# Kernel tuning notes

Measured on AMD Instinct MI355X. Metric: run time of the kernel, lower is better.

The kernel has to match this reference:

```python
import jax, jax.numpy as jnp
import numpy as np

B, C, L = 8, 64, 16384
IN, H = 64, 32


def _lstm_dir(x, wih, whh, bih, bhh):
    """Single-direction LSTM, PyTorch gate order (i, f, g, o).
    x: [B, L, H] -> hidden outputs [B, L, H]."""
    xt = jnp.transpose(x, (1, 0, 2))  # [L, B, H]
    # Precompute input contributions for all timesteps (one big GEMM).
    xg = jnp.einsum('lbh,gh->lbg', xt, wih) + bih + bhh  # [L, B, 4H]
    h0 = jnp.zeros((x.shape[0], H), x.dtype)
    c0 = jnp.zeros((x.shape[0], H), x.dtype)

    def step(carry, xg_t):
        h, c = carry
        gates = xg_t + h @ whh.T  # [B, 4H]
        i, f, g, o = jnp.split(gates, 4, axis=-1)
        i = jax.nn.sigmoid(i)
        f = jax.nn.sigmoid(f)
        g = jnp.tanh(g)
        o = jax.nn.sigmoid(o)
        c = f * c + i * g
        h = o * jnp.tanh(c)
        return (h, c), h

    _, hs = jax.lax.scan(step, (h0, c0), xg)  # hs: [L, B, H]
    return jnp.transpose(hs, (1, 0, 2))


def setup_inputs() -> dict:
    key = jax.random.key(0)
    ks = jax.random.split(key, 24)
    u = lambda k, shape, bound: jax.random.uniform(k, shape, jnp.float32, -bound, bound)
    kp = 1.0 / np.sqrt(IN)
    kh = 1.0 / np.sqrt(H)
    k2 = 1.0 / np.sqrt(2 * H)
    return {
        'x': jax.random.normal(ks[0], (B, C, L), jnp.float32),
        'proj_w': u(ks[1], (H, IN), kp), 'proj_b': u(ks[2], (H,), kp),
        'wih_f': u(ks[3], (4 * H, H), kh), 'whh_f': u(ks[4], (4 * H, H), kh),
        'bih_f': u(ks[5], (4 * H,), kh), 'bhh_f': u(ks[6], (4 * H,), kh),
        'wih_b': u(ks[7], (4 * H, H), kh), 'whh_b': u(ks[8], (4 * H, H), kh),
        'bih_b': u(ks[9], (4 * H,), kh), 'bhh_b': u(ks[10], (4 * H,), kh),
        'bc_w1': u(ks[11], (H, 2 * H), k2), 'bc_b1': u(ks[12], (H,), k2),
        'bc_w2': u(ks[13], (1, H), kh), 'bc_b2': u(ks[14], (1,), kh),
        'rc_w1': u(ks[15], (H, 2 * H), k2), 'rc_b1': u(ks[16], (H,), k2),
        'rc_w2': u(ks[17], (1, H), kh), 'rc_b2': u(ks[18], (1,), kh),
        'is_sequence': 1,
    }


def _forward(x, proj_w, proj_b, wih_f, whh_f, bih_f, bhh_f, wih_b, whh_b, bih_b, bhh_b, bc_w1, bc_b1, bc_w2, bc_b2, rc_w1, rc_b1, rc_w2, rc_b2):
    x_seq = jnp.transpose(x, (0, 2, 1))  # [B, L, C]
    projected = x_seq @ proj_w.T + proj_b  # [B, L, H]
    h_fwd = _lstm_dir(projected, wih_f, whh_f, bih_f, bhh_f)
    h_bwd = _lstm_dir(projected[:, ::-1, :], wih_b, whh_b, bih_b, bhh_b)[:, ::-1, :]
    lstm_out = jnp.concatenate([h_fwd, h_bwd], axis=-1)  # [B, L, 2H]
    # boundary classifier (Linear-ReLU-Linear-Sigmoid)
    hid = jax.nn.relu(lstm_out @ bc_w1.T + bc_b1)
    probs = jax.nn.sigmoid(hid @ bc_w2.T + bc_b2)[..., 0]  # [B, L]
    # vectorized boundary-adjust stencil (replaces the O(B*L) python loop)
    lg = probs[:, 1:-1] - probs[:, :-2]
    rg = probs[:, 1:-1] - probs[:, 2:]
    inner = jnp.where((lg < 0) & (jnp.abs(lg) > jnp.abs(rg)), -1.0,
                      jnp.where((rg < 0) & (jnp.abs(rg) > jnp.abs(lg)), 1.0, 0.0))
    adj = jnp.pad(inner.astype(probs.dtype), ((0, 0), (1, 1)))  # [B, L]
    # real classifier on mean-pooled lstm output
    pooled = lstm_out.mean(axis=1)  # [B, 2H]
    rhid = jax.nn.relu(pooled @ rc_w1.T + rc_b1)
    real = jax.nn.sigmoid(rhid @ rc_w2.T + rc_b2)  # [B, 1]
    return probs, adj, real


def reference(x, proj_w, proj_b, wih_f, whh_f, bih_f, bhh_f, wih_b, whh_b, bih_b, bhh_b, bc_w1, bc_b1, bc_w2, bc_b2, rc_w1, rc_b1, rc_w2, rc_b2, is_sequence):
    assert is_sequence  # this reference implements the is_sequence=True path
    return _forward(x, proj_w, proj_b, wih_f, whh_f, bih_f, bhh_f, wih_b, whh_b, bih_b, bhh_b, bc_w1, bc_b1, bc_w2, bc_b2, rc_w1, rc_b1, rc_w2, rc_b2)
```

## Files before the change

### kernel.cpp

```cpp
#include <hip/hip_runtime.h>

#define LSEQ 16384
#define BB 8

__device__ __forceinline__ float rcp_f(float x) { return __builtin_amdgcn_rcpf(x); }
__device__ __forceinline__ float sig_f(float x) { return rcp_f(1.f + __expf(-x)); }
__device__ __forceinline__ float rdlane(float v, int k) {
  return __int_as_float(__builtin_amdgcn_readlane(__float_as_int(v), k));
}

__device__ __forceinline__ float swap_hi(float a, float b) {
  auto r = __builtin_amdgcn_permlane32_swap(__float_as_uint(a), __float_as_uint(b), false, false);
  unsigned out[2];
  __builtin_memcpy(out, &r, 8);
  return __uint_as_float(out[1]);
}

#define PIN16(w) asm volatile("" \
  : "+v"((w)[0]), "+v"((w)[1]), "+v"((w)[2]),  "+v"((w)[3]),  \
    "+v"((w)[4]), "+v"((w)[5]), "+v"((w)[6]),  "+v"((w)[7]),  \
    "+v"((w)[8]), "+v"((w)[9]), "+v"((w)[10]), "+v"((w)[11]), \
    "+v"((w)[12]),"+v"((w)[13]),"+v"((w)[14]), "+v"((w)[15]))

__global__ __launch_bounds__(256) void k0_weights(
    const float* __restrict__ proj_w, const float* __restrict__ proj_b,
    const float* __restrict__ wih_f, const float* __restrict__ bih_f, const float* __restrict__ bhh_f,
    const float* __restrict__ wih_b, const float* __restrict__ bih_b, const float* __restrict__ bhh_b,
    float* __restrict__ Wc, float* __restrict__ Wbias) {
  int G = threadIdx.x;
  int d = G >> 7, g = G & 127;
  const float* wih = d ? wih_b : wih_f;
  const float* bih = d ? bih_b : bih_f;
  const float* bhh = d ? bhh_b : bhh_f;
  float wr[32];
  #pragma unroll
  for (int k = 0; k < 32; k += 4) {
    float4 a = *(const float4*)(wih + g * 32 + k);
    wr[k] = a.x; wr[k + 1] = a.y; wr[k + 2] = a.z; wr[k + 3] = a.w;
  }
  for (int c = 0; c < 64; ++c) {
    float s = 0.f;
    #pragma unroll
    for (int k = 0; k < 32; ++k) s = fmaf(wr[k], proj_w[k * 64 + c], s);
    Wc[c * 256 + G] = s;
  }
  float s = bih[g] + bhh[g];
  #pragma unroll
  for (int k = 0; k < 32; ++k) s = fmaf(wr[k], proj_b[k], s);
  Wbias[G] = s;
}

__global__ __launch_bounds__(256) void k1_xg(
    const float* __restrict__ x, const float* __restrict__ Wc, const float* __restrict__ Wbias,
    float* __restrict__ xg, int dsel) {
  __shared__ float lds[64 * 132];
  int tid = threadIdx.x;
  int b = blockIdx.x >> 7;
  int t0 = (blockIdx.x & 127) << 7;
  #pragma unroll
  for (int i = 0; i < 8; ++i) {
    int slot = tid + (i << 8);
    int c = slot >> 5, u4 = slot & 31;
    float4 v = *(const float4*)(x + (size_t)(b * 64 + c) * LSEQ + t0 + u4 * 4);
    *(float4*)&lds[c * 128 + u4 * 4] = v;
  }
  __syncthreads();
  int lane = tid & 63;
  int w = tid >> 6;
  int th = w >> 1;
  int tl = (th << 6) + lane;
  int gb = (w & 1) << 6;
  int gcol = __builtin_amdgcn_readfirstlane(dsel * 128 + gb);
  float acc[64];
  #pragma unroll
  for (int gg = 0; gg < 64; ++gg) acc[gg] = 0.f;
  for (int c = 0; c < 64; ++c) {
    float xv = lds[c * 128 + tl];
    #pragma unroll
    for (int gg = 0; gg < 64; ++gg)
      acc[gg] = fmaf(Wc[c * 256 + gcol + gg], xv, acc[gg]);
  }
  #pragma unroll
  for (int p = 0; p < 2; ++p) {
    __syncthreads();
    if (th == p) {
      #pragma unroll
      for (int gg = 0; gg < 64; ++gg)
        lds[(tl & 63) * 132 + gb + gg] = acc[gg] + Wbias[gcol + gg];
    }
    __syncthreads();
    float* dst = xg + (size_t)(b * LSEQ + t0 + (p << 6)) * 128;
    #pragma unroll
    for (int k = 0; k < 8; ++k) {
      int f = (tid << 2) + (k << 10);
      int trow = f >> 7, g = f & 127;
      *(float4*)(dst + f) = *(const float4*)&lds[trow * 132 + g];
    }
  }
}

template<int DIR>
__device__ __forceinline__ void scan_chunk(const float* __restrict__ whh,
                                           const float* __restrict__ xg,
                                           float* __restrict__ hbuf,
                                           int lane, int ci) {
  const int g0 = (lane < 32) ? lane : lane + 32;
  const int g1 = g0 + 32;
  float w0[32], w1[32];
  #pragma unroll
  for (int k = 0; k < 32; ++k) {
    w0[k] = whh[g0 * 32 + k];
    w1[k] = whh[g1 * 32 + k];
  }
  const float M0 = (lane < 32) ? -1.f : -2.f;
  const float S0 = (lane < 32) ? 1.f : 2.f;
  const float D0 = (lane < 32) ? 0.f : -1.f;

  const int sOwn = ci << 6;
  const int s0 = (ci == 0) ? 0 : (sOwn - 64);
  const int ow = sOwn - s0;
  const int nblk = ((sOwn + 64) - s0) >> 3;

  constexpr int ST = DIR ? -128 : 128;
  constexpr int SH = DIR ? -32 : 32;
  const float* pld = xg + (size_t)(DIR ? (LSEQ - 1 - s0) : s0) * 128;
  float* ph = hbuf + (size_t)(DIR ? (LSEQ - 1 - s0) : s0) * 32;

  float nx0[8], nx1[8];
  #pragma unroll
  for (int j = 0; j < 8; ++j) {
    nx0[j] = pld[j * ST + g0];
    nx1[j] = pld[j * ST + g1];
  }
  pld += 8 * ST;

  float h = 0.f, c = 0.f;

#define STEP(j, PREFETCH, GUARD)                                           \
  {                                                                        \
    PIN16(w0); PIN16(w0 + 16); PIN16(w1); PIN16(w1 + 16);                  \
    float c0a = nx0[j], c1a = nx1[j];                                      \
    if (PREFETCH) {                                                        \
      nx0[j] = pld[(j) * ST + g0];                                         \
      nx1[j] = pld[(j) * ST + g1];                                         \
    }                                                                      \
    float c0b = 0.f, c1b = 0.f;                                            \
    _Pragma("unroll")                                                      \
    for (int k = 0; k < 16; ++k) {                                         \
      float hA = rdlane(h, k);                                             \
      float hB = rdlane(h, k + 16);                                        \
      c0a = fmaf(hA, w0[k], c0a);                                          \
      c1a = fmaf(hA, w1[k], c1a);                                          \
      c0b = fmaf(hB, w0[k + 16], c0b);                                     \
      c1b = fmaf(hB, w1[k + 16], c1b);                                     \
    }                                                                      \
    float gx = c0a + c0b;                                                  \
    float gy = c1a + c1b;                                                  \
    float y0 = fmaf(S0, rcp_f(1.f + __expf(gx * M0)), D0);                 \
    float y1 = rcp_f(1.f + __expf(-gy));                                   \
    float b0 = swap_hi(y0, y1);                                            \
    float b1 = swap_hi(y1, y1);                                            \
    c = fmaf(y1, c, y0 * b0);                                              \
    float tc = fmaf(2.f, rcp_f(1.f + __expf(-2.f * c)), -1.f);             \
    h = b1 * tc;                                                           \
    if (GUARD) { if (lane < 32) ph[(j) * SH + lane] = h; }                 \
  }

  for (int blk = 0; blk < nblk - 1; ++blk) {
    const int sb = blk << 3;
    #pragma unroll
    for (int j = 0; j < 8; ++j) {
      STEP(j, true, sb + j >= ow);
    }
    pld += 8 * ST;
    ph += 8 * SH;
  }
  #pragma unroll
  for (int j = 0; j < 8; ++j) {
    STEP(j, false, true);
  }
#undef STEP
}

template<int DIR>
__global__ __launch_bounds__(64, 1) void k2_scan(
    const float* __restrict__ whh, const float* __restrict__ xg,
    float* __restrict__ hbuf) {
  const int lane = threadIdx.x;
  const int b = blockIdx.x >> 8;
  const int ci = blockIdx.x & 255;
  scan_chunk<DIR>(whh, xg + (size_t)b * LSEQ * 128, hbuf + (size_t)b * LSEQ * 32, lane, ci);
}

__global__ __launch_bounds__(256) void k3_probs(
    const float* __restrict__ hF, const float* __restrict__ hB,
    const float* __restrict__ w1, const float* __restrict__ b1,
    const float* __restrict__ w2, const float* __restrict__ b2,
    float* __restrict__ out, float* __restrict__ pooledP) {
  __shared__ float red[256 * 65];
  int b = blockIdx.x >> 6;
  int tile = blockIdx.x & 63;
  int t = (tile << 8) + threadIdx.x;
  const float* hf = hF + (size_t)(b * LSEQ + t) * 32;
  const float* hb = hB + (size_t)(b * LSEQ + t) * 32;
  float v[64];
  #pragma unroll
  for (int i = 0; i < 8; ++i) {
    float4 a = *(const float4*)(hf + i * 4);
    v[i * 4] = a.x; v[i * 4 + 1] = a.y; v[i * 4 + 2] = a.z; v[i * 4 + 3] = a.w;
    float4 bb = *(const float4*)(hb + i * 4);
    v[32 + i * 4] = bb.x; v[32 + i * 4 + 1] = bb.y; v[32 + i * 4 + 2] = bb.z; v[32 + i * 4 + 3] = bb.w;
  }
  float tot = b2[0];
  for (int j = 0; j < 32; ++j) {
    float s = b1[j];
    #pragma unroll
    for (int g = 0; g < 64; ++g) s = fmaf(w1[j * 64 + g], v[g], s);
    tot = fmaf(w2[j], fmaxf(s, 0.f), tot);
  }
  out[(size_t)b * LSEQ + t] = sig_f(tot);
  #pragma unroll
  for (int g = 0; g < 64; ++g) red[threadIdx.x * 65 + g] = v[g];
  __syncthreads();
  if (threadIdx.x < 64) {
    int g = threadIdx.x;
    float s = 0.f;
    for (int tt = 0; tt < 256; ++tt) s += red[tt * 65 + g];
    pooledP[(b * 64 + tile) * 64 + g] = s;
  }
}

__global__ __launch_bounds__(512) void k45_tail(
    const float* __restrict__ probs, const float* __restrict__ pooledP,
    const float* __restrict__ rw1, const float* __restrict__ rb1,
    const float* __restrict__ rw2, const float* __restrict__ rb2,
    float* __restrict__ adj, float* __restrict__ out_real) {
  __shared__ float pm[512];
  __shared__ float rh[256];
  int tid = threadIdx.x;
  if (blockIdx.x < 256) {
    int i = blockIdx.x * 512 + tid;
    int t = i & (LSEQ - 1);
    float v = 0.f;
    if (t > 0 && t < LSEQ - 1) {
      float pmv = probs[i - 1], p = probs[i], pp = probs[i + 1];
      float lg = p - pmv, rg = p - pp;
      float al = fabsf(lg), ar = fabsf(rg);
      if (lg < 0.f && al > ar) v = -1.f;
      else if (rg < 0.f && ar > al) v = 1.f;
    }
    adj[i] = v;
  } else {
    {
      int b = tid >> 6, g = tid & 63;
      float s = 0.f;
      for (int ch = 0; ch < 64; ++ch) s += pooledP[(b * 64 + ch) * 64 + g];
      pm[b * 64 + g] = s * (1.f / LSEQ);
    }
    __syncthreads();
    if (tid < 256) {
      int b = tid >> 5, j = tid & 31;
      float s = rb1[j];
      #pragma unroll
      for (int g = 0; g < 64; ++g) s = fmaf(rw1[j * 64 + g], pm[b * 64 + g], s);
      rh[b * 32 + j] = fmaxf(s, 0.f);
    }
    __syncthreads();
    if (tid < 8) {
      float s = rb2[0];
      #pragma unroll
      for (int j = 0; j < 32; ++j) s = fmaf(rw2[j], rh[tid * 32 + j], s);
      out_real[tid] = sig_f(s);
    }
  }
}

extern "C" void kernel_launch(void* const* d_in, const int* in_sizes, int n_in,
                              void* d_out, int out_size, void* d_ws, size_t ws_size,
                              hipStream_t stream) {
  const float* x      = (const float*)d_in[0];
  const float* proj_w = (const float*)d_in[1];
  const float* proj_b = (const float*)d_in[2];
  const float* wih_f  = (const float*)d_in[3];
  const float* whh_f  = (const float*)d_in[4];
  const float* bih_f  = (const float*)d_in[5];
  const float* bhh_f  = (const float*)d_in[6];
  const float* wih_b  = (const float*)d_in[7];
  const float* whh_b  = (const float*)d_in[8];
  const float* bih_b  = (const float*)d_in[9];
  const float* bhh_b  = (const float*)d_in[10];
  const float* bc_w1  = (const float*)d_in[11];
  const float* bc_b1  = (const float*)d_in[12];
  const float* bc_w2  = (const float*)d_in[13];
  const float* bc_b2  = (const float*)d_in[14];
  const float* rc_w1  = (const float*)d_in[15];
  const float* rc_b1  = (const float*)d_in[16];
  const float* rc_w2  = (const float*)d_in[17];
  const float* rc_b2  = (const float*)d_in[18];

  float* ws = (float*)d_ws;
  float* xg = ws;
  float* hF = xg + (size_t)BB * LSEQ * 128;
  float* hB = hF + (size_t)BB * LSEQ * 32;
  float* Wc = hB + (size_t)BB * LSEQ * 32;
  float* Wbias = Wc + 64 * 256;
  float* pooledP = Wbias + 256;

  float* out = (float*)d_out;
  float* probs = out;
  float* adj = out + BB * LSEQ;
  float* real = out + 2 * BB * LSEQ;

  hipLaunchKernelGGL(k0_weights, dim3(1), dim3(256), 0, stream,
                     proj_w, proj_b, wih_f, bih_f, bhh_f, wih_b, bih_b, bhh_b, Wc, Wbias);
  hipLaunchKernelGGL(k1_xg, dim3(BB * 128), dim3(256), 0, stream, x, Wc, Wbias, xg, 0);
  hipLaunchKernelGGL((k2_scan<0>), dim3(BB * 256), dim3(64), 0, stream, whh_f, xg, hF);
  hipLaunchKernelGGL(k1_xg, dim3(BB * 128), dim3(256), 0, stream, x, Wc, Wbias, xg, 1);
  hipLaunchKernelGGL((k2_scan<1>), dim3(BB * 256), dim3(64), 0, stream, whh_b, xg, hB);

  hipLaunchKernelGGL(k3_probs, dim3(BB * 64), dim3(256), 0, stream,
                     hF, hB, bc_w1, bc_b1, bc_w2, bc_b2, probs, pooledP);
  hipLaunchKernelGGL(k45_tail, dim3(257), dim3(512), 0, stream,
                     probs, pooledP, rc_w1, rc_b1, rc_w2, rc_b2, adj, real);
}
```

Measured before the change: 243.7 us.

## Run both LSTM directions concurrently and use 128-step scan chunks

Gives each direction its own input-gate buffer when the workspace is large enough. The forward and backward projection GEMMs then run as one 2048-block launch, and both direction scans run as one 2048-block launch, replacing four serialized launches. Each scan block now owns 128 timesteps instead of 64, still with a 64-step warmup, so the total redundant warmup work drops by half. The cost is lower per-direction block counts, longer sequential chains per block, and double the xg workspace; a fallback path keeps the old serialized schedule when the workspace is small.

New measurement: 246.4 us. No clear change (+1.1%).

```diff
diff --git a/kernel.cpp b/kernel.cpp
--- a/kernel.cpp
+++ b/kernel.cpp
@@ -52,11 +52,13 @@
 
 __global__ __launch_bounds__(256) void k1_xg(
     const float* __restrict__ x, const float* __restrict__ Wc, const float* __restrict__ Wbias,
-    float* __restrict__ xg, int dsel) {
+    float* __restrict__ xgF, float* __restrict__ xgB, int dselBase) {
   __shared__ float lds[64 * 132];
   int tid = threadIdx.x;
-  int b = blockIdx.x >> 7;
-  int t0 = (blockIdx.x & 127) << 7;
+  int dsel = (int)(blockIdx.x >> 10) | dselBase;
+  int bi = blockIdx.x & 1023;
+  int b = bi >> 7;
+  int t0 = (bi & 127) << 7;
   #pragma unroll
   for (int i = 0; i < 8; ++i) {
     int slot = tid + (i << 8);
@@ -80,6 +82,7 @@
     for (int gg = 0; gg < 64; ++gg)
       acc[gg] = fmaf(Wc[c * 256 + gcol + gg], xv, acc[gg]);
   }
+  float* xg = dsel ? xgB : xgF;
   #pragma unroll
   for (int p = 0; p < 2; ++p) {
     __syncthreads();
@@ -116,10 +119,10 @@
   const float S0 = (lane < 32) ? 1.f : 2.f;
   const float D0 = (lane < 32) ? 0.f : -1.f;
 
-  const int sOwn = ci << 6;
+  const int sOwn = ci << 7;
   const int s0 = (ci == 0) ? 0 : (sOwn - 64);
   const int ow = sOwn - s0;
-  const int nblk = ((sOwn + 64) - s0) >> 3;
+  const int nblk = ((sOwn + 128) - s0) >> 3;
 
   constexpr int ST = DIR ? -128 : 128;
   constexpr int SH = DIR ? -32 : 32;
@@ -182,14 +185,19 @@
 #undef STEP
 }
 
-template<int DIR>
-__global__ __launch_bounds__(64, 1) void k2_scan(
-    const float* __restrict__ whh, const float* __restrict__ xg,
-    float* __restrict__ hbuf) {
+__global__ __launch_bounds__(64, 1) void k2_dual(
+    const float* __restrict__ whh_f, const float* __restrict__ whh_b,
+    const float* __restrict__ xgF, const float* __restrict__ xgB,
+    float* __restrict__ hF, float* __restrict__ hB, int dirBase) {
   const int lane = threadIdx.x;
-  const int b = blockIdx.x >> 8;
-  const int ci = blockIdx.x & 255;
-  scan_chunk<DIR>(whh, xg + (size_t)b * LSEQ * 128, hbuf + (size_t)b * LSEQ * 32, lane, ci);
+  const int dir = (int)(blockIdx.x >> 10) + dirBase;
+  const int inner = blockIdx.x & 1023;
+  const int b = inner >> 7;
+  const int ci = inner & 127;
+  if (dir == 0)
+    scan_chunk<0>(whh_f, xgF + (size_t)b * LSEQ * 128, hF + (size_t)b * LSEQ * 32, lane, ci);
+  else
+    scan_chunk<1>(whh_b, xgB + (size_t)b * LSEQ * 128, hB + (size_t)b * LSEQ * 32, lane, ci);
 }
 
 __global__ __launch_bounds__(256) void k3_probs(
@@ -298,28 +306,54 @@
   const float* rc_w2  = (const float*)d_in[17];
   const float* rc_b2  = (const float*)d_in[18];
 
+  const size_t NXG = (size_t)BB * LSEQ * 128;
+  const size_t NH  = (size_t)BB * LSEQ * 32;
+  const size_t tail = 64 * 256 + 256 + BB * 64 * 64;
+  const size_t need_conc = (2 * NXG + 2 * NH + tail) * 4;
+
   float* ws = (float*)d_ws;
-  float* xg = ws;
-  float* hF = xg + (size_t)BB * LSEQ * 128;
-  float* hB = hF + (size_t)BB * LSEQ * 32;
-  float* Wc = hB + (size_t)BB * LSEQ * 32;
-  float* Wbias = Wc + 64 * 256;
-  float* pooledP = Wbias + 256;
-
   float* out = (float*)d_out;
   float* probs = out;
   float* adj = out + BB * LSEQ;
   float* real = out + 2 * BB * LSEQ;
 
-  hipLaunchKernelGGL(k0_weights, dim3(1), dim3(256), 0, stream,
-                     proj_w, proj_b, wih_f, bih_f, bhh_f, wih_b, bih_b, bhh_b, Wc, Wbias);
-  hipLaunchKernelGGL(k1_xg, dim3(BB * 128), dim3(256), 0, stream, x, Wc, Wbias, xg, 0);
-  hipLaunchKernelGGL((k2_scan<0>), dim3(BB * 256), dim3(64), 0, stream, whh_f, xg, hF);
-  hipLaunchKernelGGL(k1_xg, dim3(BB * 128), dim3(256), 0, stream, x, Wc, Wbias, xg, 1);
-  hipLaunchKernelGGL((k2_scan<1>), dim3(BB * 256), dim3(64), 0, stream, whh_b, xg, hB);
-
-  hipLaunchKernelGGL(k3_probs, dim3(BB * 64), dim3(256), 0, stream,
-                     hF, hB, bc_w1, bc_b1, bc_w2, bc_b2, probs, pooledP);
-  hipLaunchKernelGGL(k45_tail, dim3(257), dim3(512), 0, stream,
-                     probs, pooledP, rc_w1, rc_b1, rc_w2, rc_b2, adj, real);
-}
+  if (ws_size >= need_conc) {
+    float* xgF = ws;
+    float* xgB = xgF + NXG;
+    float* hF = xgB + NXG;
+    float* hB = hF + NH;
+    float* Wc = hB + NH;
+    float* Wbias = Wc + 64 * 256;
+    float* pooledP = Wbias + 256;
+
+    hipLaunchKernelGGL(k0_weights, dim3(1), dim3(256), 0, stream,
+                       proj_w, proj_b, wih_f, bih_f, bhh_f, wih_b, bih_b, bhh_b, Wc, Wbias);
+    hipLaunchKernelGGL(k1_xg, dim3(2048), dim3(256), 0, stream, x, Wc, Wbias, xgF, xgB, 0);
+    hipLaunchKernelGGL(k2_dual, dim3(2048), dim3(64), 0, stream,
+                       whh_f, whh_b, xgF, xgB, hF, hB, 0);
+    hipLaunchKernelGGL(k3_probs, dim3(BB * 64), dim3(256), 0, stream,
+                       hF, hB, bc_w1, bc_b1, bc_w2, bc_b2, probs, pooledP);
+    hipLaunchKernelGGL(k45_tail, dim3(257), dim3(512), 0, stream,
+                       probs, pooledP, rc_w1, rc_b1, rc_w2, rc_b2, adj, real);
+  } else {
+    float* xg = ws;
+    float* hF = xg + NXG;
+    float* hB = hF + NH;
+    float* Wc = hB + NH;
+    float* Wbias = Wc + 64 * 256;
+    float* pooledP = Wbias + 256;
+
+    hipLaunchKernelGGL(k0_weights, dim3(1), dim3(256), 0, stream,
+                       proj_w, proj_b, wih_f, bih_f, bhh_f, wih_b, bih_b, bhh_b, Wc, Wbias);
+    hipLaunchKernelGGL(k1_xg, dim3(1024), dim3(256), 0, stream, x, Wc, Wbias, xg, xg, 0);
+    hipLaunchKernelGGL(k2_dual, dim3(1024), dim3(64), 0, stream,
+                       whh_f, whh_b, xg, xg, hF, hB, 0);
+    hipLaunchKernelGGL(k1_xg, dim3(1024), dim3(256), 0, stream, x, Wc, Wbias, xg, xg, 1);
+    hipLaunchKernelGGL(k2_dual, dim3(1024), dim3(64), 0, stream,
+                       whh_f, whh_b, xg, xg, hF, hB, 1);
+    hipLaunchKernelGGL(k3_probs, dim3(BB * 64), dim3(256), 0, stream,
+                       hF, hB, bc_w1, bc_b1, bc_w2, bc_b2, probs, pooledP);
+    hipLaunchKernelGGL(k45_tail, dim3(257), dim3(512), 0, stream,
+                       probs, pooledP, rc_w1, rc_b1, rc_w2, rc_b2, adj, real);
+  }
+}
```
